# Kernel optimization log

Measured on AMD Instinct MI355X. Metric: run time of the kernel, lower is better.

## Reference

```python
import jax, jax.numpy as jnp
import numpy as np

EMBED_DIM = 1024
NUM_HEADS = 16
HEAD_DIM = EMBED_DIM // NUM_HEADS
SCALE = HEAD_DIM ** -0.5


def setup_inputs() -> dict:
    key = jax.random.key(0)
    ks = jax.random.split(key, 9)
    B, S, D = 32, 577, EMBED_DIM
    std = 1.0 / np.sqrt(D)
    inp = {
        "hidden_states": jax.random.normal(ks[0], (B, S, D), dtype=jnp.float32),
        "q_w": jax.random.normal(ks[1], (D, D), dtype=jnp.float32) * std,
        "q_b": jax.random.normal(ks[2], (D,), dtype=jnp.float32) * 0.01,
        "k_w": jax.random.normal(ks[3], (D, D), dtype=jnp.float32) * std,
        "k_b": jax.random.normal(ks[4], (D,), dtype=jnp.float32) * 0.01,
        "v_w": jax.random.normal(ks[5], (D, D), dtype=jnp.float32) * std,
        "v_b": jax.random.normal(ks[6], (D,), dtype=jnp.float32) * 0.01,
        "o_w": jax.random.normal(ks[7], (D, D), dtype=jnp.float32) * std,
        "o_b": jax.random.normal(ks[8], (D,), dtype=jnp.float32) * 0.01,
    }
    return inp


def reference(hidden_states, q_w, q_b, k_w, k_b, v_w, v_b, o_w, o_b):
    B, S, D = hidden_states.shape
    H, Dh = NUM_HEADS, HEAD_DIM

    def proj(w, b):
        # torch Linear: x @ w.T + b ; reshape to [B, H, S, Dh]
        y = jnp.einsum('bsd,ed->bse', hidden_states, w) + b
        return y.reshape(B, S, H, Dh).transpose(0, 2, 1, 3)

    q = proj(q_w, q_b)
    k = proj(k_w, k_b)
    v = proj(v_w, v_b)

    scores = jnp.einsum('bhqd,bhkd->bhqk', q * SCALE, k)  # [B,H,S,S]
    attn = jax.nn.softmax(scores, axis=-1)
    out = jnp.einsum('bhqk,bhkd->bhqd', attn, v)  # [B,H,S,Dh]
    out = out.transpose(0, 2, 1, 3).reshape(B, S, D)
    return jnp.einsum('bsd,ed->bse', out, o_w) + o_b
```

## Files before the change

kernel.cpp:

```cpp
#include <hip/hip_runtime.h>
#include <hip/hip_bf16.h>
#include <stdint.h>

#define B_   32
#define S_   577
#define SP   640
#define D_   1024
#define H_   16
#define DH   64
#define BH_  (B_*H_)
#define M_   (B_*S_)
#define MP2  18688
#define SCALE_ 0.125f
#define LOG2E_ 1.44269504088896f

typedef __bf16 bf16;
typedef __bf16 bf16x8 __attribute__((ext_vector_type(8)));
typedef __bf16 bf16x4 __attribute__((ext_vector_type(4)));
typedef float  f32x4  __attribute__((ext_vector_type(4)));

__device__ __forceinline__ void gload16(const bf16* g, bf16* l) {
    __builtin_amdgcn_global_load_lds((__attribute__((address_space(1))) void*)g,
                                     (__attribute__((address_space(3))) void*)l, 16, 0, 0);
}

__global__ void cast_kernel(const float* __restrict__ in, bf16* __restrict__ out, int n4) {
    int i = blockIdx.x * blockDim.x + threadIdx.x;
    if (i >= n4) return;
    float4 v = ((const float4*)in)[i];
    bf16x4 o;
    o[0] = (bf16)v.x; o[1] = (bf16)v.y; o[2] = (bf16)v.z; o[3] = (bf16)v.w;
    ((bf16x4*)out)[i] = o;
}

__global__ void cast4_kernel(const float* __restrict__ w0, const float* __restrict__ w1,
                             const float* __restrict__ w2, const float* __restrict__ w3,
                             bf16* __restrict__ o0, bf16* __restrict__ o1,
                             bf16* __restrict__ o2, bf16* __restrict__ o3) {
    int i = blockIdx.x * blockDim.x + threadIdx.x;
    int seg = i >> 18, r = i & 262143;
    const float* in = (seg == 0) ? w0 : (seg == 1) ? w1 : (seg == 2) ? w2 : w3;
    bf16* out       = (seg == 0) ? o0 : (seg == 1) ? o1 : (seg == 2) ? o2 : o3;
    float4 v = ((const float4*)in)[r];
    bf16x4 o;
    o[0] = (bf16)v.x; o[1] = (bf16)v.y; o[2] = (bf16)v.z; o[3] = (bf16)v.w;
    ((bf16x4*)out)[r] = o;
}

__device__ __forceinline__ void stage256(const bf16* __restrict__ A, const bf16* __restrict__ B,
                                         int m0, int n0, int K, int kt, bf16* SMbuf) {
    const int tid = threadIdx.x;
    const int wave = tid >> 6;
    #pragma unroll
    for (int ld = 0; ld < 4; ++ld) {
        int ci  = (ld & 1) * 512 + tid;
        int lr  = ci >> 3;
        int ch  = (ci & 7) ^ (lr & 7);
        int row = lr * 2 + (ch >> 2);
        int kof = (ch & 3) * 8;
        const bf16* g = ((ld < 2) ? (A + (size_t)(m0 + row) * K)
                                  : (B + (size_t)(n0 + row) * K)) + kt * 32 + kof;
        bf16* l = SMbuf + (ld < 2 ? 0 : 8192) + (size_t)((ld & 1) * 512 + wave * 64) * 8;
        gload16(g, l);
    }
}

__device__ __forceinline__ void compute256(const bf16* SMbuf, f32x4 acc[8][4],
                                           int wm, int wn, int r16, int c4) {
    bf16x8 bq[4];
    #pragma unroll
    for (int j = 0; j < 4; ++j) {
        int row = wn * 64 + j * 16 + r16;
        int lr  = row >> 1;
        int cc  = (((row & 1) << 2) + c4) ^ (lr & 7);
        bq[j] = *(const bf16x8*)(SMbuf + 8192 + lr * 64 + cc * 8);
    }
    #pragma unroll
    for (int i = 0; i < 8; ++i) {
        int row = wm * 128 + i * 16 + r16;
        int lr  = row >> 1;
        int cc  = (((row & 1) << 2) + c4) ^ (lr & 7);
        bf16x8 a = *(const bf16x8*)(SMbuf + lr * 64 + cc * 8);
        #pragma unroll
        for (int j = 0; j < 4; ++j)
            acc[i][j] = __builtin_amdgcn_mfma_f32_16x16x32_bf16(a, bq[j], acc[i][j], 0, 0, 0);
    }
}

__device__ __forceinline__ void gemm_mainloop(const bf16* __restrict__ A, const bf16* __restrict__ Bw,
                                              int m0, int n0, bf16* SM, f32x4 acc[8][4],
                                              int wm, int wn, int r16, int c4) {
    stage256(A, Bw, m0, n0, 1024, 0, SM);
    __syncthreads();
    for (int kt = 0; kt < 32; ++kt) {
        if (kt < 31) stage256(A, Bw, m0, n0, 1024, kt + 1, SM + ((kt + 1) & 1) * 16384);
        compute256(SM + (kt & 1) * 16384, acc, wm, wn, r16, c4);
        __syncthreads();
    }
}

__global__ __launch_bounds__(512, 2) void gemm_qkv(const bf16* __restrict__ A, const bf16* __restrict__ Bw,
                                                   const float* __restrict__ qb, const float* __restrict__ kb,
                                                   const float* __restrict__ vb,
                                                   bf16* __restrict__ qk, bf16* __restrict__ vT) {
    __shared__ __align__(16) char SMc[66304];
    bf16* SM = (bf16*)SMc;
    const int bx = blockIdx.x;
    const int bm = bx / 12, bn = bx % 12;
    const int m0 = bm * 256, n0 = bn * 256;
    const int tid = threadIdx.x;
    const int lane = tid & 63, wave = tid >> 6;
    const int wm = wave >> 2, wn = wave & 3;
    const int r16 = lane & 15, c4 = lane >> 4;

    f32x4 acc[8][4];
    #pragma unroll
    for (int i = 0; i < 8; ++i)
        #pragma unroll
        for (int j = 0; j < 4; ++j)
            #pragma unroll
            for (int r = 0; r < 4; ++r) acc[i][j][r] = 0.0f;

    gemm_mainloop(A, Bw, m0, n0, SM, acc, wm, wn, r16, c4);

    if (bn < 8) {
        const float* barr = (bn < 4) ? qb : kb;
        const float mul = (bn < 4) ? SCALE_ * LOG2E_ : 1.0f;
        #pragma unroll
        for (int j = 0; j < 4; ++j) {
            int n = n0 + wn * 64 + j * 16 + r16;
            float bias = barr[n & 1023];
            #pragma unroll
            for (int i = 0; i < 8; ++i) {
                #pragma unroll
                for (int r = 0; r < 4; ++r) {
                    int m = m0 + wm * 128 + i * 16 + c4 * 4 + r;
                    if (m < M_) qk[(size_t)m * 2048 + n] = (bf16)((acc[i][j][r] + bias) * mul);
                }
            }
        }
    } else {
        const int bnp = bn - 8;
        bf16* Ts = (bf16*)SMc;
        #pragma unroll
        for (int mh = 0; mh < 2; ++mh) {
            if (wm == mh) {
                #pragma unroll
                for (int j = 0; j < 4; ++j) {
                    int nl = wn * 64 + j * 16 + r16;
                    float bias = vb[bnp * 256 + nl];
                    #pragma unroll
                    for (int i = 0; i < 8; ++i) {
                        #pragma unroll
                        for (int r = 0; r < 4; ++r) {
                            int tr = i * 16 + c4 * 4 + r;
                            Ts[tr * 259 + nl] = (bf16)(acc[i][j][r] + bias);
                        }
                    }
                }
            }
            __syncthreads();
            {
                int ml = tid & 127, nh = tid >> 7;
                int gm = m0 + mh * 128 + ml;
                if (gm < M_) {
                    unsigned bb = (unsigned)gm / 577u, s = (unsigned)gm - bb * 577u;
                    bf16* dst = vT + ((size_t)((bb * 16 + bnp * 4 + nh) * 64)) * SP + s;
                    const bf16* src = Ts + ml * 259 + nh * 64;
                    #pragma unroll 8
                    for (int j = 0; j < 64; ++j) dst[(size_t)j * SP] = src[j];
                }
            }
            __syncthreads();
        }
    }
}

__global__ __launch_bounds__(512, 2) void gemm_out(const bf16* __restrict__ A, const bf16* __restrict__ Bw,
                                                   const float* __restrict__ ob, float* __restrict__ out) {
    __shared__ __align__(16) bf16 SM[2 * 16384];
    const int bx = blockIdx.x;
    const int bm = bx >> 2, bn = bx & 3;
    const int m0 = bm * 256, n0 = bn * 256;
    const int tid = threadIdx.x;
    const int lane = tid & 63, wave = tid >> 6;
    const int wm = wave >> 2, wn = wave & 3;
    const int r16 = lane & 15, c4 = lane >> 4;

    f32x4 acc[8][4];
    #pragma unroll
    for (int i = 0; i < 8; ++i)
        #pragma unroll
        for (int j = 0; j < 4; ++j)
            #pragma unroll
            for (int r = 0; r < 4; ++r) acc[i][j][r] = 0.0f;

    gemm_mainloop(A, Bw, m0, n0, SM, acc, wm, wn, r16, c4);

    #pragma unroll
    for (int j = 0; j < 4; ++j) {
        int n = n0 + wn * 64 + j * 16 + r16;
        float bias = ob[n];
        #pragma unroll
        for (int i = 0; i < 8; ++i) {
            #pragma unroll
            for (int r = 0; r < 4; ++r) {
                int m = m0 + wm * 128 + i * 16 + c4 * 4 + r;
                if (m < M_) out[(size_t)m * 1024 + n] = acc[i][j][r] + bias;
            }
        }
    }
}

__global__ __launch_bounds__(256) void attn_kernel(const bf16* __restrict__ qk,
                                                   const bf16* __restrict__ vT, bf16* __restrict__ obuf) {
    __shared__ __align__(16) bf16 KV[2][2][4096];
    __shared__ __align__(16) char Pls[4 * 2 * 2048];
    const int orig = blockIdx.x;
    const int xcd = orig & 7;
    const int t   = orig >> 3;
    const int qt  = t % 5, bhg = t / 5;
    const int bh  = bhg * 8 + xcd;
    const int b   = bh >> 4, h = bh & 15;
    const int tid = threadIdx.x;
    const int lane = tid & 63, wave = tid >> 6;
    const int r16 = lane & 15, c4 = lane >> 4;
    const int q0  = qt * 128 + wave * 32;
    const int swz = (r16 & 7) << 4;

    const bf16* qp = qk + (size_t)(b * 577) * 2048 + h * 64;
    const bf16* kp = qp + 1024;
    const bf16* vp = vT + (size_t)bh * 64 * SP;

    bf16x8 aq[2][2];
    #pragma unroll
    for (int qf = 0; qf < 2; ++qf)
        #pragma unroll
        for (int c = 0; c < 2; ++c)
            aq[qf][c] = *(const bf16x8*)(qp + (size_t)(q0 + qf * 16 + r16) * 2048 + c * 32 + c4 * 8);

    float mi[2] = {-3.0e38f, -3.0e38f};
    float li[2] = {0.0f, 0.0f};
    f32x4 accO[2][4];
    #pragma unroll
    for (int qf = 0; qf < 2; ++qf)
        #pragma unroll
        for (int nt = 0; nt < 4; ++nt)
            #pragma unroll
            for (int r = 0; r < 4; ++r) accO[qf][nt][r] = 0.0f;

    char* pbase = Pls + wave * 4096 + r16 * 128;

    auto stageKV = [&](int kt, int buf) {
        #pragma unroll
        for (int half = 0; half < 2; ++half) {
            int li  = half * 256 + tid;
            int row = li >> 3;
            int ch  = (li & 7) ^ (row & 7);
            bf16* lk = &KV[buf][0][(size_t)(half * 256 + wave * 64) * 8];
            bf16* lv = &KV[buf][1][(size_t)(half * 256 + wave * 64) * 8];
            gload16(kp + (size_t)(kt * 64 + row) * 2048 + ch * 8, lk);
            gload16(vp + (size_t)row * SP + kt * 64 + ch * 8, lv);
        }
    };

    stageKV(0, 0);
    __syncthreads();

    for (int kt = 0; kt < 10; ++kt) {
        const int buf = kt & 1;
        if (kt < 9) stageKV(kt + 1, buf ^ 1);

        bf16x8 kf[4][2];
        #pragma unroll
        for (int nt = 0; nt < 4; ++nt)
            #pragma unroll
            for (int c = 0; c < 2; ++c) {
                int row = nt * 16 + r16;
                int cc  = (c * 4 + c4) ^ (row & 7);
                kf[nt][c] = *(const bf16x8*)(&KV[buf][0][row * 64 + cc * 8]);
            }
        f32x4 sc[2][4];
        #pragma unroll
        for (int qf = 0; qf < 2; ++qf)
            #pragma unroll
            for (int nt = 0; nt < 4; ++nt) {
                f32x4 z = {0.0f, 0.0f, 0.0f, 0.0f};
                z = __builtin_amdgcn_mfma_f32_16x16x32_bf16(kf[nt][0], aq[qf][0], z, 0, 0, 0);
                sc[qf][nt] = __builtin_amdgcn_mfma_f32_16x16x32_bf16(kf[nt][1], aq[qf][1], z, 0, 0, 0);
            }

        #pragma unroll
        for (int qf = 0; qf < 2; ++qf) {
            if (kt == 9) {
                #pragma unroll
                for (int nt = 0; nt < 4; ++nt)
                    #pragma unroll
                    for (int r = 0; r < 4; ++r)
                        if (576 + nt * 16 + c4 * 4 + r >= S_) sc[qf][nt][r] = -3.0e38f;
            }
            float pmax = sc[qf][0][0];
            #pragma unroll
            for (int nt = 0; nt < 4; ++nt)
                #pragma unroll
                for (int r = 0; r < 4; ++r) pmax = fmaxf(pmax, sc[qf][nt][r]);
            pmax = fmaxf(pmax, __shfl_xor(pmax, 16));
            pmax = fmaxf(pmax, __shfl_xor(pmax, 32));

            const bool vrow = (q0 + qf * 16 + r16) < S_;
            int ok = (!vrow) || (pmax <= mi[qf] + 8.0f);
            if (!__all(ok)) {
                float mnew = fmaxf(mi[qf], pmax);
                float fsc  = __builtin_amdgcn_exp2f(mi[qf] - mnew);
                mi[qf] = mnew;
                li[qf] *= fsc;
                float fs0 = __shfl(fsc, c4 * 4 + 0);
                float fs1 = __shfl(fsc, c4 * 4 + 1);
                float fs2 = __shfl(fsc, c4 * 4 + 2);
                float fs3 = __shfl(fsc, c4 * 4 + 3);
                #pragma unroll
                for (int nt = 0; nt < 4; ++nt) {
                    accO[qf][nt][0] *= fs0; accO[qf][nt][1] *= fs1;
                    accO[qf][nt][2] *= fs2; accO[qf][nt][3] *= fs3;
                }
            }
            float p[4][4];
            float rs = 0.0f;
            #pragma unroll
            for (int nt = 0; nt < 4; ++nt)
                #pragma unroll
                for (int r = 0; r < 4; ++r) {
                    p[nt][r] = __builtin_amdgcn_exp2f(sc[qf][nt][r] - mi[qf]);
                    rs += p[nt][r];
                }
            rs += __shfl_xor(rs, 16);
            rs += __shfl_xor(rs, 32);
            li[qf] += rs;
            #pragma unroll
            for (int nt = 0; nt < 4; ++nt) {
                bf16x4 pk;
                pk[0] = (bf16)p[nt][0]; pk[1] = (bf16)p[nt][1];
                pk[2] = (bf16)p[nt][2]; pk[3] = (bf16)p[nt][3];
                *(bf16x4*)(pbase + qf * 2048 + ((nt * 32 + c4 * 8) ^ swz)) = pk;
            }
        }

        bf16x8 vf[4][2];
        #pragma unroll
        for (int ntd = 0; ntd < 4; ++ntd)
            #pragma unroll
            for (int kk = 0; kk < 2; ++kk) {
                int row = ntd * 16 + r16;
                int cc  = (kk * 4 + c4) ^ (row & 7);
                vf[ntd][kk] = *(const bf16x8*)(&KV[buf][1][row * 64 + cc * 8]);
            }
        #pragma unroll
        for (int qf = 0; qf < 2; ++qf) {
            bf16x8 pf[2];
            #pragma unroll
            for (int kk = 0; kk < 2; ++kk)
                pf[kk] = *(const bf16x8*)(pbase + qf * 2048 + ((kk * 64 + c4 * 16) ^ swz));
            #pragma unroll
            for (int ntd = 0; ntd < 4; ++ntd)
                #pragma unroll
                for (int kk = 0; kk < 2; ++kk)
                    accO[qf][ntd] = __builtin_amdgcn_mfma_f32_16x16x32_bf16(pf[kk], vf[ntd][kk], accO[qf][ntd], 0, 0, 0);
        }

        __syncthreads();
    }

    #pragma unroll
    for (int qf = 0; qf < 2; ++qf) {
        float inv = 1.0f / li[qf];
        float rl0 = __shfl(inv, c4 * 4 + 0);
        float rl1 = __shfl(inv, c4 * 4 + 1);
        float rl2 = __shfl(inv, c4 * 4 + 2);
        float rl3 = __shfl(inv, c4 * 4 + 3);
        #pragma unroll
        for (int ntd = 0; ntd < 4; ++ntd) {
            #pragma unroll
            for (int r = 0; r < 4; ++r) {
                int s = q0 + qf * 16 + c4 * 4 + r;
                if (s < S_) {
                    float rl = (r == 0) ? rl0 : (r == 1) ? rl1 : (r == 2) ? rl2 : rl3;
                    obuf[((size_t)(b * S_ + s)) * 1024 + h * 64 + ntd * 16 + r16] =
                        (bf16)(accO[qf][ntd][r] * rl);
                }
            }
        }
    }
}

extern "C" void kernel_launch(void* const* d_in, const int* in_sizes, int n_in,
                              void* d_out, int out_size, void* d_ws, size_t ws_size,
                              hipStream_t stream) {
    const float* hs = (const float*)d_in[0];
    const float* qw = (const float*)d_in[1];
    const float* qb = (const float*)d_in[2];
    const float* kw = (const float*)d_in[3];
    const float* kb = (const float*)d_in[4];
    const float* vw = (const float*)d_in[5];
    const float* vb = (const float*)d_in[6];
    const float* ow = (const float*)d_in[7];
    const float* ob = (const float*)d_in[8];

    char* ws = (char*)d_ws;
    size_t off = 0;
    auto alloc = [&](size_t bytes) { void* p = ws + off; off += (bytes + 255) & ~255UL; return p; };
    bf16* hsA  = (bf16*)alloc((size_t)MP2 * 1024 * 2);
    bf16* wqkv = (bf16*)alloc((size_t)3072 * 1024 * 2);
    bf16* wo   = (bf16*)alloc((size_t)1024 * 1024 * 2);
    bf16* qk   = (bf16*)alloc((size_t)MP2 * 2048 * 2);
    bf16* vT   = (bf16*)alloc((size_t)BH_ * 64 * SP * 2);

    hipMemsetAsync(vT, 0, (size_t)BH_ * 64 * SP * 2, stream);

    int n4h = M_ * 1024 / 4;
    cast_kernel<<<(n4h + 255) / 256, 256, 0, stream>>>(hs, hsA, n4h);
    cast4_kernel<<<4096, 256, 0, stream>>>(qw, kw, vw, ow,
                                           wqkv, wqkv + 1048576, wqkv + 2097152, wo);

    gemm_qkv<<<73 * 12, 512, 0, stream>>>(hsA, wqkv, qb, kb, vb, qk, vT);
    attn_kernel<<<2560, 256, 0, stream>>>(qk, vT, hsA);
    gemm_out<<<73 * 4, 512, 0, stream>>>(hsA, wo, ob, (float*)d_out);
}
```

Measured before the change: 390.6 us.

## Deepen GEMM mainloop to four-buffer prefetch with split-phase MFMA scheduling

Replaces the double-buffered GEMM main loop with a four-slot LDS ring that prefetches three k-tiles ahead. Each k-tile is split into two MFMA halves, with the A and B loads for a future tile issued between them. Explicit vmcnt/lgkmcnt waits, raw s_barrier and s_setprio are meant to better hide global-load latency behind matrix math. LDS per block grows to 128 KB, which likely stops two blocks from sharing a CU and cuts occupancy.

```diff
diff --git a/kernel.cpp b/kernel.cpp
--- a/kernel.cpp
+++ b/kernel.cpp
@@ -18,6 +18,14 @@
 typedef __bf16 bf16x8 __attribute__((ext_vector_type(8)));
 typedef __bf16 bf16x4 __attribute__((ext_vector_type(4)));
 typedef float  f32x4  __attribute__((ext_vector_type(4)));
+
+#define BARRIER() __builtin_amdgcn_s_barrier()
+
+template<int N> __device__ __forceinline__ void vmwait() {
+    if constexpr (N == 8) asm volatile("s_waitcnt vmcnt(8)" ::: "memory");
+    else if constexpr (N == 4) asm volatile("s_waitcnt vmcnt(4)" ::: "memory");
+    else if constexpr (N == 0) asm volatile("s_waitcnt vmcnt(0)" ::: "memory");
+}
 
 __device__ __forceinline__ void gload16(const bf16* g, bf16* l) {
     __builtin_amdgcn_global_load_lds((__attribute__((address_space(1))) void*)g,
@@ -47,63 +55,102 @@
     ((bf16x4*)out)[r] = o;
 }
 
-__device__ __forceinline__ void stage256(const bf16* __restrict__ A, const bf16* __restrict__ B,
-                                         int m0, int n0, int K, int kt, bf16* SMbuf) {
-    const int tid = threadIdx.x;
-    const int wave = tid >> 6;
-    #pragma unroll
-    for (int ld = 0; ld < 4; ++ld) {
-        int ci  = (ld & 1) * 512 + tid;
-        int lr  = ci >> 3;
-        int ch  = (ci & 7) ^ (lr & 7);
-        int row = lr * 2 + (ch >> 2);
-        int kof = (ch & 3) * 8;
-        const bf16* g = ((ld < 2) ? (A + (size_t)(m0 + row) * K)
-                                  : (B + (size_t)(n0 + row) * K)) + kt * 32 + kof;
-        bf16* l = SMbuf + (ld < 2 ? 0 : 8192) + (size_t)((ld & 1) * 512 + wave * 64) * 8;
-        gload16(g, l);
-    }
-}
-
-__device__ __forceinline__ void compute256(const bf16* SMbuf, f32x4 acc[8][4],
-                                           int wm, int wn, int r16, int c4) {
-    bf16x8 bq[4];
+__device__ __forceinline__ void stageA3(const bf16* __restrict__ A, int m0, int kt,
+                                        bf16* nxt, int tid, int wave) {
+    #pragma unroll
+    for (int ld = 0; ld < 2; ++ld) {
+        int ci = ld * 512 + tid, lr = ci >> 3, ch = (ci & 7) ^ (lr & 7);
+        int row = lr * 2 + (ch >> 2), kof = (ch & 3) * 8;
+        gload16(A + (size_t)(m0 + row) * 1024 + kt * 32 + kof,
+                nxt + (size_t)(ld * 512 + wave * 64) * 8);
+    }
+}
+__device__ __forceinline__ void stageB3(const bf16* __restrict__ Bw, int n0, int kt,
+                                        bf16* nxt, int tid, int wave) {
+    #pragma unroll
+    for (int ld = 0; ld < 2; ++ld) {
+        int ci = ld * 512 + tid, lr = ci >> 3, ch = (ci & 7) ^ (lr & 7);
+        int row = lr * 2 + (ch >> 2), kof = (ch & 3) * 8;
+        gload16(Bw + (size_t)(n0 + row) * 1024 + kt * 32 + kof,
+                nxt + 8192 + (size_t)(ld * 512 + wave * 64) * 8);
+    }
+}
+
+template<int VMN, bool STG>
+__device__ __forceinline__ void ktile(const bf16* __restrict__ A, const bf16* __restrict__ Bw,
+                                      int m0, int n0, int kt, bf16* SM, f32x4 acc[8][4],
+                                      int wm, int wn, int r16, int c4, int tid, int wave) {
+    bf16* cur = SM + (kt & 3) * 16384;
+    bf16* nxt = SM + ((kt + 3) & 3) * 16384;
+    bf16x8 af[4], bfr[4];
+
+    #pragma unroll
+    for (int i = 0; i < 4; ++i) {
+        int row = wm * 128 + i * 16 + r16, lr = row >> 1;
+        int cc = (((row & 1) << 2) + c4) ^ (lr & 7);
+        af[i] = *(const bf16x8*)(cur + lr * 64 + cc * 8);
+    }
     #pragma unroll
     for (int j = 0; j < 4; ++j) {
-        int row = wn * 64 + j * 16 + r16;
-        int lr  = row >> 1;
-        int cc  = (((row & 1) << 2) + c4) ^ (lr & 7);
-        bq[j] = *(const bf16x8*)(SMbuf + 8192 + lr * 64 + cc * 8);
-    }
-    #pragma unroll
-    for (int i = 0; i < 8; ++i) {
-        int row = wm * 128 + i * 16 + r16;
-        int lr  = row >> 1;
-        int cc  = (((row & 1) << 2) + c4) ^ (lr & 7);
-        bf16x8 a = *(const bf16x8*)(SMbuf + lr * 64 + cc * 8);
+        int row = wn * 64 + j * 16 + r16, lr = row >> 1;
+        int cc = (((row & 1) << 2) + c4) ^ (lr & 7);
+        bfr[j] = *(const bf16x8*)(cur + 8192 + lr * 64 + cc * 8);
+    }
+    if (STG) stageA3(A, m0, kt + 3, nxt, tid, wave);
+    BARRIER();
+    asm volatile("s_waitcnt lgkmcnt(0)" ::: "memory");
+    __builtin_amdgcn_s_setprio(1);
+    #pragma unroll
+    for (int i = 0; i < 4; ++i)
         #pragma unroll
         for (int j = 0; j < 4; ++j)
-            acc[i][j] = __builtin_amdgcn_mfma_f32_16x16x32_bf16(a, bq[j], acc[i][j], 0, 0, 0);
-    }
+            acc[i][j] = __builtin_amdgcn_mfma_f32_16x16x32_bf16(af[i], bfr[j], acc[i][j], 0, 0, 0);
+    __builtin_amdgcn_s_setprio(0);
+    BARRIER();
+
+    #pragma unroll
+    for (int i = 0; i < 4; ++i) {
+        int row = wm * 128 + (4 + i) * 16 + r16, lr = row >> 1;
+        int cc = (((row & 1) << 2) + c4) ^ (lr & 7);
+        af[i] = *(const bf16x8*)(cur + lr * 64 + cc * 8);
+    }
+    if (STG) stageB3(Bw, n0, kt + 3, nxt, tid, wave);
+    vmwait<VMN>();
+    BARRIER();
+    asm volatile("s_waitcnt lgkmcnt(0)" ::: "memory");
+    __builtin_amdgcn_s_setprio(1);
+    #pragma unroll
+    for (int i = 0; i < 4; ++i)
+        #pragma unroll
+        for (int j = 0; j < 4; ++j)
+            acc[4 + i][j] = __builtin_amdgcn_mfma_f32_16x16x32_bf16(af[i], bfr[j], acc[4 + i][j], 0, 0, 0);
+    __builtin_amdgcn_s_setprio(0);
+    BARRIER();
 }
 
 __device__ __forceinline__ void gemm_mainloop(const bf16* __restrict__ A, const bf16* __restrict__ Bw,
                                               int m0, int n0, bf16* SM, f32x4 acc[8][4],
-                                              int wm, int wn, int r16, int c4) {
-    stage256(A, Bw, m0, n0, 1024, 0, SM);
-    __syncthreads();
-    for (int kt = 0; kt < 32; ++kt) {
-        if (kt < 31) stage256(A, Bw, m0, n0, 1024, kt + 1, SM + ((kt + 1) & 1) * 16384);
-        compute256(SM + (kt & 1) * 16384, acc, wm, wn, r16, c4);
-        __syncthreads();
-    }
+                                              int wm, int wn, int r16, int c4, int tid, int wave) {
+    #pragma unroll
+    for (int kt = 0; kt < 3; ++kt) {
+        bf16* buf = SM + kt * 16384;
+        stageA3(A, m0, kt, buf, tid, wave);
+        stageB3(Bw, n0, kt, buf, tid, wave);
+    }
+    vmwait<8>();
+    BARRIER();
+    for (int kt = 0; kt < 29; ++kt)
+        ktile<8, true>(A, Bw, m0, n0, kt, SM, acc, wm, wn, r16, c4, tid, wave);
+    ktile<4, false>(A, Bw, m0, n0, 29, SM, acc, wm, wn, r16, c4, tid, wave);
+    ktile<0, false>(A, Bw, m0, n0, 30, SM, acc, wm, wn, r16, c4, tid, wave);
+    ktile<-1, false>(A, Bw, m0, n0, 31, SM, acc, wm, wn, r16, c4, tid, wave);
 }
 
 __global__ __launch_bounds__(512, 2) void gemm_qkv(const bf16* __restrict__ A, const bf16* __restrict__ Bw,
                                                    const float* __restrict__ qb, const float* __restrict__ kb,
                                                    const float* __restrict__ vb,
                                                    bf16* __restrict__ qk, bf16* __restrict__ vT) {
-    __shared__ __align__(16) char SMc[66304];
+    __shared__ __align__(16) char SMc[131072];
     bf16* SM = (bf16*)SMc;
     const int bx = blockIdx.x;
     const int bm = bx / 12, bn = bx % 12;
@@ -121,7 +168,8 @@
             #pragma unroll
             for (int r = 0; r < 4; ++r) acc[i][j][r] = 0.0f;
 
-    gemm_mainloop(A, Bw, m0, n0, SM, acc, wm, wn, r16, c4);
+    gemm_mainloop(A, Bw, m0, n0, SM, acc, wm, wn, r16, c4, tid, wave);
+    __syncthreads();
 
     if (bn < 8) {
         const float* barr = (bn < 4) ? qb : kb;
@@ -178,7 +226,7 @@
 
 __global__ __launch_bounds__(512, 2) void gemm_out(const bf16* __restrict__ A, const bf16* __restrict__ Bw,
                                                    const float* __restrict__ ob, float* __restrict__ out) {
-    __shared__ __align__(16) bf16 SM[2 * 16384];
+    __shared__ __align__(16) bf16 SM[4 * 16384];
     const int bx = blockIdx.x;
     const int bm = bx >> 2, bn = bx & 3;
     const int m0 = bm * 256, n0 = bn * 256;
@@ -195,7 +243,7 @@
             #pragma unroll
             for (int r = 0; r < 4; ++r) acc[i][j][r] = 0.0f;
 
-    gemm_mainloop(A, Bw, m0, n0, SM, acc, wm, wn, r16, c4);
+    gemm_mainloop(A, Bw, m0, n0, SM, acc, wm, wn, r16, c4, tid, wave);
 
     #pragma unroll
     for (int j = 0; j < 4; ++j) {
```

After: 385.2 us. About the same (-1.4%).
